# Kernel tuning notes

Hardware: AMD Instinct MI355X
Metric: run time of the kernel (lower is better)

## Reference

```python
import jax, jax.numpy as jnp
import numpy as np

DIM = 1024
HEADS = 16
DIM_HEAD = 64
INNER = HEADS * DIM_HEAD  # 1024
EPS = 1e-5


def setup_inputs() -> dict:
    key = jax.random.key(0)
    ks = jax.random.split(key, 5)
    x = jax.random.normal(ks[0], (4, 2048, DIM), dtype=jnp.float32)
    ln_gamma = jnp.ones((DIM,), dtype=jnp.float32)
    ln_beta = jnp.zeros((DIM,), dtype=jnp.float32)
    # nn.Linear weights ~ U(-1/sqrt(fan_in), 1/sqrt(fan_in)); stored as (out, in) in torch,
    # here kept as (in, out) for x @ W.
    lim = 1.0 / np.sqrt(DIM)
    w_qkv = jax.random.uniform(ks[1], (DIM, 3 * INNER), minval=-lim, maxval=lim, dtype=jnp.float32)
    lim2 = 1.0 / np.sqrt(INNER)
    w_out = jax.random.uniform(ks[2], (INNER, DIM), minval=-lim2, maxval=lim2, dtype=jnp.float32)
    return {"x": x, "ln_gamma": ln_gamma, "ln_beta": ln_beta, "w_qkv": w_qkv, "w_out": w_out}


def reference(x, ln_gamma, ln_beta, w_qkv, w_out):
    b, n, d = x.shape
    # LayerNorm
    mu = jnp.mean(x, axis=-1, keepdims=True)
    var = jnp.mean(jnp.square(x - mu), axis=-1, keepdims=True)
    xn = (x - mu) * jax.lax.rsqrt(var + EPS) * ln_gamma + ln_beta
    # QKV projection
    qkv = xn @ w_qkv  # (b, n, 3*inner)
    q, k, v = jnp.split(qkv, 3, axis=-1)
    def to_heads(t):
        return t.reshape(b, n, HEADS, DIM_HEAD).transpose(0, 2, 1, 3)  # (b,h,n,dh)
    q, k, v = to_heads(q), to_heads(k), to_heads(v)
    scale = DIM_HEAD ** -0.5
    scores = jnp.einsum('bhqd,bhkd->bhqk', q, k) * scale
    causal = jnp.tril(jnp.ones((n, n), dtype=bool))
    scores = jnp.where(causal, scores, -jnp.inf)
    probs = jax.nn.softmax(scores, axis=-1)
    out = jnp.einsum('bhqk,bhkd->bhqd', probs, v)
    out = out.transpose(0, 2, 1, 3).reshape(b, n, INNER)
    return out @ w_out
```

## Files before the change

### kernel.cpp

```cpp
#include <hip/hip_runtime.h>
#include <hip/hip_bf16.h>

#define DIM 1024
#define HEADS 16
#define DH 64
#define SEQ 2048
#define BATCH 4
#define ROWS (BATCH * SEQ)
#define NQKV (3 * DIM)

typedef __attribute__((ext_vector_type(8))) __bf16 bf16x8;
typedef __attribute__((ext_vector_type(4))) __bf16 bf16x4;
typedef __attribute__((ext_vector_type(4))) float f32x4;

__device__ inline void gload16(const void* g, void* l) {
  __builtin_amdgcn_global_load_lds(
      (const __attribute__((address_space(1))) void*)g,
      (__attribute__((address_space(3))) void*)l, 16, 0, 0);
}

__device__ inline float fast_exp2(float x) {
#if __has_builtin(__builtin_amdgcn_exp2f)
  return __builtin_amdgcn_exp2f(x);
#else
  return exp2f(x);
#endif
}

__global__ __launch_bounds__(256) void ln_tc(
    const float* __restrict__ x, const float* __restrict__ gamma,
    const float* __restrict__ beta, __bf16* __restrict__ xnb,
    const float* __restrict__ wq, const float* __restrict__ wo,
    __bf16* __restrict__ qT, __bf16* __restrict__ oT) {
  __shared__ float red1[4], red2[4];
  __shared__ float tile[32][33];
  const int bid = blockIdx.x;
  const int tid = threadIdx.x;
  if (bid < ROWS) {
    const float4* xr = (const float4*)(x + (size_t)bid * DIM);
    float4 v = xr[tid];
    float s1 = v.x + v.y + v.z + v.w;
    float s2 = v.x * v.x + v.y * v.y + v.z * v.z + v.w * v.w;
#pragma unroll
    for (int d = 32; d > 0; d >>= 1) {
      s1 += __shfl_xor(s1, d);
      s2 += __shfl_xor(s2, d);
    }
    const int wave = tid >> 6, lane = tid & 63;
    if (lane == 0) { red1[wave] = s1; red2[wave] = s2; }
    __syncthreads();
    s1 = red1[0] + red1[1] + red1[2] + red1[3];
    s2 = red2[0] + red2[1] + red2[2] + red2[3];
    const float mean = s1 * (1.0f / DIM);
    const float var = s2 * (1.0f / DIM) - mean * mean;
    const float rstd = rsqrtf(var + 1e-5f);
    float4 g = ((const float4*)gamma)[tid];
    float4 b = ((const float4*)beta)[tid];
    bf16x4 o;
    o[0] = (__bf16)((v.x - mean) * rstd * g.x + b.x);
    o[1] = (__bf16)((v.y - mean) * rstd * g.y + b.y);
    o[2] = (__bf16)((v.z - mean) * rstd * g.z + b.z);
    o[3] = (__bf16)((v.w - mean) * rstd * g.w + b.w);
    *(bf16x4*)(xnb + (size_t)bid * DIM + tid * 4) = o;
  } else {
    const int id2 = bid - ROWS;
    int bx = id2 & 127;
    const int by = id2 >> 7;
    const int tx = tid & 31, ty = tid >> 5;
    const float* in;
    __bf16* out;
    int cols;
    if (bx < 96) {
      in = wq; out = qT; cols = NQKV;
    } else {
      in = wo; out = oT; cols = DIM; bx -= 96;
    }
    const int c0 = bx * 32, r0 = by * 32;
#pragma unroll
    for (int rr = ty; rr < 32; rr += 8)
      tile[rr][tx] = in[(size_t)(r0 + rr) * cols + c0 + tx];
    __syncthreads();
#pragma unroll
    for (int rr = ty; rr < 32; rr += 8)
      out[(size_t)(c0 + rr) * DIM + r0 + tx] = (__bf16)tile[tx][rr];
  }
}

template <int MODE>
__global__ __launch_bounds__(512, 1) void gemmP(
    const __bf16* __restrict__ A, const __bf16* __restrict__ Bt, const int K,
    const int N, float* __restrict__ Cout, __bf16* __restrict__ qb,
    __bf16* __restrict__ kb, __bf16* __restrict__ vtb) {
  __shared__ __bf16 As[3][2][128 * 64];
  __shared__ __bf16 Bs[3][128 * 64];
  const int tid = threadIdx.x;
  const int wave = tid >> 6, lane = tid & 63;
  const int quad = lane >> 4, l16 = lane & 15;
  const int wm = wave >> 2, wn = wave & 3;

  const size_t tileM = (size_t)blockIdx.x * 256;
  const size_t tileN = (size_t)blockIdx.y * 128;
  const int sel = (MODE == 1) ? (int)(tileN >> 10) : 0;
  const bool vmode = (MODE == 1) && (sel == 2);

  f32x4 acc[8][2];
#pragma unroll
  for (int a = 0; a < 8; ++a)
#pragma unroll
    for (int b = 0; b < 2; ++b) acc[a][b] = (f32x4){0.f, 0.f, 0.f, 0.f};

  const __bf16* Abase = A + tileM * (size_t)K;
  const __bf16* Bbase = Bt + tileN * (size_t)K;

  const int slr = tid >> 3, sc = tid & 7;
  const int scol = (sc ^ (slr & 7)) << 3;

  auto stageA = [&](int buf, int h, int kt) {
    const size_t col = (size_t)(kt << 6) + scol;
#pragma unroll
    for (int p = 0; p < 2; ++p) {
      const int gr = p * 128 + h * 64 + slr;
      const int lr = p * 64 + slr;
      gload16(Abase + (size_t)gr * K + col, &As[buf][h][lr * 64 + sc * 8]);
    }
  };
  auto stageB = [&](int buf, int kt) {
    const size_t col = (size_t)(kt << 6) + scol;
#pragma unroll
    for (int p = 0; p < 2; ++p) {
      const int lr = p * 64 + slr;
      gload16(Bbase + (size_t)lr * K + col, &Bs[buf][lr * 64 + sc * 8]);
    }
  };
  auto stageTile = [&](int buf, int kt) {
    stageA(buf, 0, kt);
    stageB(buf, kt);
    stageA(buf, 1, kt);
  };

  const int rpc = quad ^ (l16 & 7);
  auto ldA = [&](int buf, int mt, int ks) -> bf16x8 {
    const int lr = wm * 64 + (mt & 3) * 16 + l16;
    return *(const bf16x8*)&As[buf][mt >> 2][lr * 64 + ((rpc ^ (ks << 2)) << 3)];
  };
  auto ldB = [&](int buf, int nt, int ks) -> bf16x8 {
    const int lr = wn * 32 + nt * 16 + l16;
    return *(const bf16x8*)&Bs[buf][lr * 64 + ((rpc ^ (ks << 2)) << 3)];
  };

  auto cluster = [&](const bf16x8* af, bf16x8 bf0, bf16x8 bf1, int mb) {
    __builtin_amdgcn_s_setprio(1);
    if (vmode) {
#pragma unroll
      for (int mt = 0; mt < 4; ++mt) {
        acc[mb + mt][0] = __builtin_amdgcn_mfma_f32_16x16x32_bf16(
            af[mt], bf0, acc[mb + mt][0], 0, 0, 0);
        acc[mb + mt][1] = __builtin_amdgcn_mfma_f32_16x16x32_bf16(
            af[mt], bf1, acc[mb + mt][1], 0, 0, 0);
      }
    } else {
#pragma unroll
      for (int mt = 0; mt < 4; ++mt) {
        acc[mb + mt][0] = __builtin_amdgcn_mfma_f32_16x16x32_bf16(
            bf0, af[mt], acc[mb + mt][0], 0, 0, 0);
        acc[mb + mt][1] = __builtin_amdgcn_mfma_f32_16x16x32_bf16(
            bf1, af[mt], acc[mb + mt][1], 0, 0, 0);
      }
    }
    __builtin_amdgcn_s_setprio(0);
  };

  stageTile(0, 0);
  stageTile(1, 1);

  const int NT = K >> 6;
  int bufc = 0;
  bf16x8 af[4], b00, b01, b10, b11;

  for (int t = 0; t < NT; ++t) {
    if (t < NT - 1)
      asm volatile("s_waitcnt vmcnt(6)" ::: "memory");
    else
      asm volatile("s_waitcnt vmcnt(0)" ::: "memory");
    __builtin_amdgcn_s_barrier();
    asm volatile("" ::: "memory");
    __builtin_amdgcn_sched_barrier(0);

    if (t + 2 < NT) {
      const int sb = bufc + 2 >= 3 ? bufc - 1 : bufc + 2;
      stageTile(sb, t + 2);
    }

#pragma unroll
    for (int mt = 0; mt < 4; ++mt) af[mt] = ldA(bufc, mt, 0);
    b00 = ldB(bufc, 0, 0);
    b01 = ldB(bufc, 1, 0);
    cluster(af, b00, b01, 0);
#pragma unroll
    for (int mt = 0; mt < 4; ++mt) af[mt] = ldA(bufc, mt, 1);
    b10 = ldB(bufc, 0, 1);
    b11 = ldB(bufc, 1, 1);
    cluster(af, b10, b11, 0);
#pragma unroll
    for (int mt = 0; mt < 4; ++mt) af[mt] = ldA(bufc, 4 + mt, 0);
    cluster(af, b00, b01, 4);
#pragma unroll
    for (int mt = 0; mt < 4; ++mt) af[mt] = ldA(bufc, 4 + mt, 1);
    cluster(af, b10, b11, 4);

    bufc = bufc == 2 ? 0 : bufc + 1;
  }

  if (MODE == 0) {
#pragma unroll
    for (int mt = 0; mt < 8; ++mt) {
      const size_t m = tileM + wm * 128 + mt * 16 + l16;
#pragma unroll
      for (int nt = 0; nt < 2; ++nt) {
        const size_t n0 = tileN + wn * 32 + nt * 16 + quad * 4;
        *(f32x4*)&Cout[m * (size_t)N + n0] = acc[mt][nt];
      }
    }
  } else if (sel < 2) {
    __bf16* dst = (sel == 0) ? qb : kb;
#pragma unroll
    for (int mt = 0; mt < 8; ++mt) {
      const size_t m = tileM + wm * 128 + mt * 16 + l16;
      const int b = (int)(m >> 11), seq = (int)(m & 2047);
#pragma unroll
      for (int nt = 0; nt < 2; ++nt) {
        const int c = (int)(tileN & 1023) + wn * 32 + nt * 16 + quad * 4;
        const int head = c >> 6, dh = c & 63;
        bf16x4 pk;
#pragma unroll
        for (int r = 0; r < 4; ++r) pk[r] = (__bf16)acc[mt][nt][r];
        *(bf16x4*)&dst[(((size_t)b * HEADS + head) * SEQ + seq) * DH + dh] = pk;
      }
    }
  } else {
#pragma unroll
    for (int nt = 0; nt < 2; ++nt) {
      const int c = (int)(tileN & 1023) + wn * 32 + nt * 16 + l16;
      const int head = c >> 6, dh = c & 63;
#pragma unroll
      for (int mt = 0; mt < 8; ++mt) {
        const size_t m0 = tileM + wm * 128 + mt * 16 + quad * 4;
        const int b = (int)(m0 >> 11), seq = (int)(m0 & 2047);
        bf16x4 pk;
#pragma unroll
        for (int r = 0; r < 4; ++r) pk[r] = (__bf16)acc[mt][nt][r];
        *(bf16x4*)&vtb[(((size_t)b * HEADS + head) * DH + dh) * SEQ + seq] = pk;
      }
    }
  }
}

__global__ __launch_bounds__(256, 4) void attn_kernel(
    const __bf16* __restrict__ qb, const __bf16* __restrict__ kb,
    const __bf16* __restrict__ vtb, __bf16* __restrict__ ob) {
  const int bh = blockIdx.x;
  const int by = blockIdx.y;
  const int tid = threadIdx.x;
  const int wave = tid >> 6, lane = tid & 63;
  const int quad = lane >> 4, l16 = lane & 15;

  __shared__ __bf16 Ks[2][64 * 64];
  __shared__ __bf16 Vs[2][64 * 64];
  __shared__ __bf16 Ps[4][16 * 36];

  const __bf16* kg = kb + (size_t)bh * SEQ * DH;
  const __bf16* vg = vtb + (size_t)bh * DH * SEQ;

  const int i1 = by, i2 = 31 - by;
  const int T = 33;

  const int kr = lane >> 3, kc = lane & 7;

  auto stage = [&](int buf, int j) {
#pragma unroll
    for (int p = 0; p < 2; ++p) {
      const int rbase = wave * 16 + p * 8;
      const int row = rbase + kr;
      gload16(kg + (size_t)(j * 64 + row) * DH + ((kc ^ (row & 7)) << 3),
              &Ks[buf][rbase * 64]);
      gload16(vg + (size_t)row * SEQ + j * 64 + ((kc ^ (row & 7)) << 3),
              &Vs[buf][rbase * 64]);
    }
  };

  const float QSCALE = 0.125f * 1.44269504088896f;
  bf16x8 qf[2];
  auto load_q = [&](int i) {
    const __bf16* qbase = qb + ((size_t)bh * SEQ + (size_t)i * 64 + wave * 16) * DH;
#pragma unroll
    for (int ks = 0; ks < 2; ++ks) {
      bf16x8 v = *(const bf16x8*)(qbase + l16 * DH + ks * 32 + quad * 8);
#pragma unroll
      for (int e = 0; e < 8; ++e) v[e] = (__bf16)((float)v[e] * QSCALE);
      qf[ks] = v;
    }
  };

  float m_i, l_i;
  f32x4 o_acc[4];
  auto reset_state = [&]() {
    m_i = -1e30f;
    l_i = 0.f;
#pragma unroll
    for (int md = 0; md < 4; ++md) o_acc[md] = (f32x4){0.f, 0.f, 0.f, 0.f};
  };
  const int b_out = bh >> 4, h_out = bh & 15;
  auto epilogue = [&](int i) {
    float lsum = l_i;
    lsum += __shfl_xor(lsum, 16);
    lsum += __shfl_xor(lsum, 32);
    const float inv = __builtin_amdgcn_rcpf(lsum);
    const int seq = i * 64 + wave * 16 + l16;
    __bf16* dst = ob + ((size_t)b_out * SEQ + seq) * DIM + h_out * DH;
#pragma unroll
    for (int md = 0; md < 4; ++md) {
      bf16x4 pk;
#pragma unroll
      for (int r = 0; r < 4; ++r) pk[r] = (__bf16)(o_acc[md][r] * inv);
      *(bf16x4*)(dst + md * 16 + quad * 4) = pk;
    }
  };

  load_q(i1);
  reset_state();
  stage(0, 0);

  for (int t = 0; t < T; ++t) {
    __syncthreads();
    if (t + 1 < T) {
      const int jn = (t + 1 <= by) ? (t + 1) : (t - by);
      stage((t + 1) & 1, jn);
    }
    const int buf = t & 1;
    const int i = (t <= by) ? i1 : i2;
    const int j = (t <= by) ? t : (t - by - 1);
    const bool diag = (j == i);

    f32x4 sa[4];
#pragma unroll
    for (int nt = 0; nt < 4; ++nt) sa[nt] = (f32x4){0.f, 0.f, 0.f, 0.f};
    __builtin_amdgcn_s_setprio(1);
#pragma unroll
    for (int nt = 0; nt < 4; ++nt)
#pragma unroll
      for (int ks = 0; ks < 2; ++ks) {
        bf16x8 kf = *(const bf16x8*)&Ks[buf][(nt * 16 + l16) * 64 +
                                            (((ks * 4 + quad) ^ (l16 & 7)) << 3)];
        sa[nt] = __builtin_amdgcn_mfma_f32_16x16x32_bf16(kf, qf[ks], sa[nt], 0, 0, 0);
      }
    __builtin_amdgcn_s_setprio(0);

    if (diag) {
      const int qrl = wave * 16 + l16;
#pragma unroll
      for (int nt = 0; nt < 4; ++nt)
#pragma unroll
        for (int r = 0; r < 4; ++r) {
          const int kvl = nt * 16 + quad * 4 + r;
          if (kvl > qrl) sa[nt][r] = -1e30f;
        }
    }

    {
      float mx = -1e30f;
#pragma unroll
      for (int nt = 0; nt < 4; ++nt) {
        const float a0 = fmaxf(fmaxf(sa[nt][0], sa[nt][1]), sa[nt][2]);
        mx = fmaxf(mx, fmaxf(a0, sa[nt][3]));
      }
      mx = fmaxf(mx, __shfl_xor(mx, 16));
      mx = fmaxf(mx, __shfl_xor(mx, 32));
      if (__all(mx - m_i <= 8.f)) {
        float rs = 0.f;
#pragma unroll
        for (int nt = 0; nt < 4; ++nt)
#pragma unroll
          for (int r = 0; r < 4; ++r) {
            const float p = fast_exp2(sa[nt][r] - m_i);
            sa[nt][r] = p;
            rs += p;
          }
        l_i += rs;
      } else {
        const float mnew = fmaxf(m_i, mx);
        const float alpha = fast_exp2(m_i - mnew);
        m_i = mnew;
        float rs = 0.f;
#pragma unroll
        for (int nt = 0; nt < 4; ++nt)
#pragma unroll
          for (int r = 0; r < 4; ++r) {
            const float p = fast_exp2(sa[nt][r] - mnew);
            sa[nt][r] = p;
            rs += p;
          }
        l_i = l_i * alpha + rs;
#pragma unroll
        for (int md = 0; md < 4; ++md)
#pragma unroll
          for (int r = 0; r < 4; ++r) o_acc[md][r] *= alpha;
      }
    }

#pragma unroll
    for (int c = 0; c < 2; ++c) {
#pragma unroll
      for (int ntl = 0; ntl < 2; ++ntl) {
        const int nt = c * 2 + ntl;
        bf16x4 pk;
#pragma unroll
        for (int r = 0; r < 4; ++r) pk[r] = (__bf16)sa[nt][r];
        *(bf16x4*)&Ps[wave][l16 * 36 + ntl * 16 + quad * 4] = pk;
      }
      bf16x8 pf = *(const bf16x8*)&Ps[wave][l16 * 36 + quad * 8];
      __builtin_amdgcn_s_setprio(1);
#pragma unroll
      for (int md = 0; md < 4; ++md) {
        bf16x8 vf = *(const bf16x8*)&Vs[buf][(md * 16 + l16) * 64 +
                                            (((c * 4 + quad) ^ (l16 & 7)) << 3)];
        o_acc[md] = __builtin_amdgcn_mfma_f32_16x16x32_bf16(vf, pf, o_acc[md], 0, 0, 0);
      }
      __builtin_amdgcn_s_setprio(0);
    }

    if (t == by) {
      epilogue(i1);
      reset_state();
      load_q(i2);
    }
  }
  epilogue(i2);
}

extern "C" void kernel_launch(void* const* d_in, const int* in_sizes, int n_in,
                              void* d_out, int out_size, void* d_ws, size_t ws_size,
                              hipStream_t stream) {
  const float* x = (const float*)d_in[0];
  const float* gamma = (const float*)d_in[1];
  const float* beta = (const float*)d_in[2];
  const float* w_qkv = (const float*)d_in[3];
  const float* w_out = (const float*)d_in[4];
  float* out = (float*)d_out;

  char* ws = (char*)d_ws;
  const size_t MB = 1024 * 1024;
  __bf16* xnb = (__bf16*)ws;
  __bf16* wqkvT = (__bf16*)(ws + 16 * MB);
  __bf16* woutT = (__bf16*)(ws + 24 * MB);
  __bf16* qbuf = (__bf16*)(ws + 32 * MB);
  __bf16* kbuf = (__bf16*)(ws + 48 * MB);
  __bf16* vtbuf = (__bf16*)(ws + 64 * MB);
  __bf16* attnb = xnb;

  ln_tc<<<ROWS + 4096, 256, 0, stream>>>(x, gamma, beta, xnb, w_qkv, w_out,
                                         wqkvT, woutT);
  gemmP<1><<<dim3(ROWS / 256, NQKV / 128), 512, 0, stream>>>(
      xnb, wqkvT, DIM, NQKV, nullptr, qbuf, kbuf, vtbuf);
  attn_kernel<<<dim3(BATCH * HEADS, 16), 256, 0, stream>>>(qbuf, kbuf, vtbuf, attnb);
  gemmP<0><<<dim3(ROWS / 256, DIM / 128), 512, 0, stream>>>(
      attnb, woutT, DIM, DIM, out, nullptr, nullptr, nullptr);
}
```

Measured before the change: 267.5 us.

## Load K and V fragments directly from global memory instead of LDS staging

Removes the double-buffered LDS staging of K and V tiles via global_load_lds and the per-iteration block barrier. Each wave now reads its own K and V MFMA fragments straight from global memory, relying on L1/L2 caching. This drops the synchronisation and the LDS footprint, which may raise occupancy. In exchange, each of the four waves repeats the K/V global reads, and the loads are no longer prefetched one tile ahead, so their latency is exposed.

Result: slower. 442.0 us (+65.2%).

```diff
diff --git a/kernel.cpp b/kernel.cpp
--- a/kernel.cpp
+++ b/kernel.cpp
@@ -264,8 +264,6 @@
   const int wave = tid >> 6, lane = tid & 63;
   const int quad = lane >> 4, l16 = lane & 15;
 
-  __shared__ __bf16 Ks[2][64 * 64];
-  __shared__ __bf16 Vs[2][64 * 64];
   __shared__ __bf16 Ps[4][16 * 36];
 
   const __bf16* kg = kb + (size_t)bh * SEQ * DH;
@@ -273,20 +271,6 @@
 
   const int i1 = by, i2 = 31 - by;
   const int T = 33;
-
-  const int kr = lane >> 3, kc = lane & 7;
-
-  auto stage = [&](int buf, int j) {
-#pragma unroll
-    for (int p = 0; p < 2; ++p) {
-      const int rbase = wave * 16 + p * 8;
-      const int row = rbase + kr;
-      gload16(kg + (size_t)(j * 64 + row) * DH + ((kc ^ (row & 7)) << 3),
-              &Ks[buf][rbase * 64]);
-      gload16(vg + (size_t)row * SEQ + j * 64 + ((kc ^ (row & 7)) << 3),
-              &Vs[buf][rbase * 64]);
-    }
-  };
 
   const float QSCALE = 0.125f * 1.44269504088896f;
   bf16x8 qf[2];
@@ -328,19 +312,21 @@
 
   load_q(i1);
   reset_state();
-  stage(0, 0);
 
   for (int t = 0; t < T; ++t) {
-    __syncthreads();
-    if (t + 1 < T) {
-      const int jn = (t + 1 <= by) ? (t + 1) : (t - by);
-      stage((t + 1) & 1, jn);
-    }
-    const int buf = t & 1;
     const int i = (t <= by) ? i1 : i2;
     const int j = (t <= by) ? t : (t - by - 1);
     const bool diag = (j == i);
 
+    bf16x8 kf[4][2];
+#pragma unroll
+    for (int nt = 0; nt < 4; ++nt)
+#pragma unroll
+      for (int ks = 0; ks < 2; ++ks)
+        kf[nt][ks] = *(const bf16x8*)(kg +
+                                      (size_t)(j * 64 + nt * 16 + l16) * DH +
+                                      (ks * 4 + quad) * 8);
+
     f32x4 sa[4];
 #pragma unroll
     for (int nt = 0; nt < 4; ++nt) sa[nt] = (f32x4){0.f, 0.f, 0.f, 0.f};
@@ -348,11 +334,9 @@
 #pragma unroll
     for (int nt = 0; nt < 4; ++nt)
 #pragma unroll
-      for (int ks = 0; ks < 2; ++ks) {
-        bf16x8 kf = *(const bf16x8*)&Ks[buf][(nt * 16 + l16) * 64 +
-                                            (((ks * 4 + quad) ^ (l16 & 7)) << 3)];
-        sa[nt] = __builtin_amdgcn_mfma_f32_16x16x32_bf16(kf, qf[ks], sa[nt], 0, 0, 0);
-      }
+      for (int ks = 0; ks < 2; ++ks)
+        sa[nt] = __builtin_amdgcn_mfma_f32_16x16x32_bf16(kf[nt][ks], qf[ks],
+                                                         sa[nt], 0, 0, 0);
     __builtin_amdgcn_s_setprio(0);
 
     if (diag) {
@@ -421,8 +405,8 @@
       __builtin_amdgcn_s_setprio(1);
 #pragma unroll
       for (int md = 0; md < 4; ++md) {
-        bf16x8 vf = *(const bf16x8*)&Vs[buf][(md * 16 + l16) * 64 +
-                                            (((c * 4 + quad) ^ (l16 & 7)) << 3)];
+        bf16x8 vf = *(const bf16x8*)(vg + (size_t)(md * 16 + l16) * SEQ +
+                                     (size_t)j * 64 + (c * 4 + quad) * 8);
         o_acc[md] = __builtin_amdgcn_mfma_f32_16x16x32_bf16(vf, pf, o_acc[md], 0, 0, 0);
       }
       __builtin_amdgcn_s_setprio(0);
```
